# Performance work log

Measured on AMD Instinct MI355X. Metric: run time of the kernel, lower is better.

## Reference

```python
import jax, jax.numpy as jnp
import numpy as np


def _exp_levels(dx, depth):
    """Tensor-algebra exponential of a single increment dx [B, C]:
    level j is dx^{(x) j} / j!, flattened to [B, C^j]."""
    B = dx.shape[0]
    levels = [dx]
    for j in range(2, depth + 1):
        levels.append((jnp.einsum('bi,bj->bij', levels[-1], dx) / j).reshape(B, -1))
    return levels


def _chen_step(levels, dx, depth):
    """Chen's identity: sig(path * segment) = sig(path) (x) exp(dx).
    levels: tuple of [B, C^k] for k=1..depth. dx: [B, C]."""
    B = dx.shape[0]
    exps = _exp_levels(dx, depth)
    new = []
    for k in range(1, depth + 1):
        acc = levels[k - 1] + exps[k - 1]  # A_k * 1  +  1 * E_k
        for j in range(1, k):
            # A_{k-j} (x) E_j, flattened: [B, C^{k-j}] x [B, C^j] -> [B, C^k]
            acc = acc + jnp.einsum('bi,bj->bij', levels[k - j - 1], exps[j - 1]).reshape(B, -1)
        new.append(acc)
    return tuple(new)


def setup_inputs() -> dict:
    key = jax.random.key(0)
    path = jax.random.normal(key, (64, 512, 10), dtype=jnp.float32)
    return {"path": path, "depth": 4}


def reference(path, depth):
    # signature(path, depth, stream=False, basepoint=False, inverse=False,
    #           initial=None, scalar_term=False)
    dx = path[:, 1:] - path[:, :-1]  # [B, L-1, C] increments
    B = path.shape[0]
    # Initialise with the signature of the first segment: exp(dx_0).
    init = tuple(_exp_levels(dx[:, 0], depth))
    # Fold remaining segments via Chen's relation (a sequential scan; the
    # original's batch-trick is just a reassociation of this same product).
    dx_rest = jnp.swapaxes(dx[:, 1:], 0, 1)  # [L-2, B, C]

    def step(carry, d):
        return _chen_step(carry, d, depth), None

    carry, _ = jax.lax.scan(step, init, dx_rest)
    # Concatenate levels: output [B, C + C^2 + ... + C^depth]
    return jnp.concatenate(carry, axis=-1)
```

## Files before the change

### kernel.cpp

```cpp
#include <hip/hip_runtime.h>


#define CH      10
#define NSTEPS  511
#define SIGSZ   11110
#define WSSEG   11112
#define NSEG    8
#define SEGLEN  64
#define TRP     68

__global__ __launch_bounds__(256)
void sig_partial(const float* __restrict__ path, float* __restrict__ ws) {
    __shared__ __align__(16) float rowL[SEGLEN * 12];
    __shared__ __align__(16) float trL[CH * TRP];

    const int tid = threadIdx.x;
    const int bx  = blockIdx.x;
    const int b   = bx >> 3;
    const int seg = bx & 7;
    const int s0  = seg * SEGLEN;

    const float* p = path + (size_t)b * (512 * CH) + s0 * CH;
    for (int e = tid; e < SEGLEN * CH; e += 256) {
        const int s = e / CH;
        const int c = e - s * CH;
        float v = 0.f;
        if (s0 + s < NSTEPS) v = p[e + CH] - p[e];
        rowL[s * 12 + c] = v;
        trL[c * TRP + s] = v;
    }
    __syncthreads();

    const int half = tid >> 7;
    const int ij   = tid & 127;
    if (ij < 100) {
        const int ci = ij / 10;
        const int cj = ij - ci * 10;

        float a1 = 0.f, a2 = 0.f;
        float a3[5];
        float a4[5][10];
        #pragma unroll
        for (int m = 0; m < 5; ++m) {
            a3[m] = 0.f;
            #pragma unroll
            for (int l = 0; l < 10; ++l) a4[m][l] = 0.f;
        }

        const float* ti = trL + ci * TRP;
        const float* tj = trL + cj * TRP;

        auto run = [&](auto hc) {
            constexpr int H = decltype(hc)::value;
            for (int s4 = 0; s4 < SEGLEN; s4 += 4) {
                const float4 vi = *(const float4*)(ti + s4);
                const float4 vj = *(const float4*)(tj + s4);
                const float* rp = rowL + s4 * 12;
                #pragma unroll
                for (int u = 0; u < 4; ++u) {
                    const float4 d0 = *(const float4*)(rp + u * 12);
                    const float4 d1 = *(const float4*)(rp + u * 12 + 4);
                    const float2 d2 = *(const float2*)(rp + u * 12 + 8);
                    const float dxi = (u == 0) ? vi.x : (u == 1) ? vi.y
                                     : (u == 2) ? vi.z : vi.w;
                    const float dxj = (u == 0) ? vj.x : (u == 1) ? vj.y
                                     : (u == 2) ? vj.z : vj.w;

                    const float p1 = a1 * (1.f / 6.f) + dxi * (1.f / 24.f);
                    const float q1 = a1 * 0.5f        + dxi * (1.f / 6.f);
                    const float r1 = a1               + dxi * 0.5f;
                    const float p2 = a2 * 0.5f + p1 * dxj;
                    const float q2 = a2        + q1 * dxj;
                    a2 += r1 * dxj;
                    a1 += dxi;

                    const float dk0 = H ? d1.y : d0.x;
                    const float dk1 = H ? d1.z : d0.y;
                    const float dk2 = H ? d1.w : d0.z;
                    const float dk3 = H ? d2.x : d0.w;
                    const float dk4 = H ? d2.y : d1.x;

                    const float p30 = a3[0] + p2 * dk0;  a3[0] += q2 * dk0;
                    const float p31 = a3[1] + p2 * dk1;  a3[1] += q2 * dk1;
                    const float p32 = a3[2] + p2 * dk2;  a3[2] += q2 * dk2;
                    const float p33 = a3[3] + p2 * dk3;  a3[3] += q2 * dk3;
                    const float p34 = a3[4] + p2 * dk4;  a3[4] += q2 * dk4;

                    #pragma unroll
                    for (int m = 0; m < 5; ++m) {
                        const float p3 = (m == 0) ? p30 : (m == 1) ? p31
                                        : (m == 2) ? p32 : (m == 3) ? p33 : p34;
                        a4[m][0] += p3 * d0.x; a4[m][1] += p3 * d0.y;
                        a4[m][2] += p3 * d0.z; a4[m][3] += p3 * d0.w;
                        a4[m][4] += p3 * d1.x; a4[m][5] += p3 * d1.y;
                        a4[m][6] += p3 * d1.z; a4[m][7] += p3 * d1.w;
                        a4[m][8] += p3 * d2.x; a4[m][9] += p3 * d2.y;
                    }
                }
            }
        };
        if (half == 0) run(std::integral_constant<int, 0>{});
        else           run(std::integral_constant<int, 1>{});

        const int k0 = half * 5;
        float* ob = ws + (size_t)(b * NSEG + seg) * WSSEG;
        #pragma unroll
        for (int m = 0; m < 5; ++m) {
            const int id = ci * 100 + cj * 10 + k0 + m;
            float* o4 = ob + 1110 + id * 10;
            #pragma unroll
            for (int l = 0; l < 10; ++l) o4[l] = a4[m][l];
            ob[110 + id] = a3[m];
        }
        if (half == 0)            ob[10 + ci * 10 + cj] = a2;
        if (half == 0 && cj == 0) ob[ci] = a1;
    }
}

__global__ __launch_bounds__(256)
void sig_combine(const float* __restrict__ ws, float* __restrict__ out) {
    __shared__ float B[1110];

    const int tid  = threadIdx.x;
    const int b    = blockIdx.x >> 2;
    const int part = blockIdx.x & 3;
    const int id   = part * 256 + tid;
    const bool valid = (id < 1000);

    const int ci = id / 100;
    const int cj = (id / 10) % 10;
    const int ck = id % 10;

    const float* w0 = ws + (size_t)b * NSEG * WSSEG;

    float a1 = 0.f, a2 = 0.f, a3 = 0.f;
    float a4[10];
    #pragma unroll
    for (int l = 0; l < 10; ++l) a4[l] = 0.f;
    if (valid) {
        a1 = w0[ci];
        a2 = w0[10 + ci * 10 + cj];
        a3 = w0[110 + id];
        #pragma unroll
        for (int l = 0; l < 10; ++l) a4[l] = w0[1110 + id * 10 + l];
    }

    for (int s = 1; s < NSEG; ++s) {
        const float* wb = w0 + (size_t)s * WSSEG;
        __syncthreads();
        for (int e = tid; e < 1110; e += 256) B[e] = wb[e];
        __syncthreads();

        if (valid) {
            const float b1i   = B[ci];
            const float b1j   = B[cj];
            const float b1k   = B[ck];
            const float b2_ij = B[10 + ci * 10 + cj];
            const float b2_jk = B[10 + cj * 10 + ck];
            const float b3ijk = B[110 + id];

            float b4v[10];
            #pragma unroll
            for (int l = 0; l < 10; ++l) b4v[l] = wb[1110 + id * 10 + l];

            #pragma unroll
            for (int l = 0; l < 10; ++l)
                a4[l] += a3 * B[l] + a2 * B[10 + ck * 10 + l]
                       + a1 * B[110 + (cj * 10 + ck) * 10 + l] + b4v[l];
            a3 += a2 * b1k + a1 * b2_jk + b3ijk;
            a2 += a1 * b1j + b2_ij;
            a1 += b1i;
        }
    }

    if (valid) {
        float* ob = out + (size_t)b * SIGSZ;
        float* o4 = ob + 1110 + id * 10;
        #pragma unroll
        for (int l = 0; l < 10; ++l) o4[l] = a4[l];
        ob[110 + id] = a3;
        if (ck == 0)            ob[10 + ci * 10 + cj] = a2;
        if (ck == 0 && cj == 0) ob[ci] = a1;
    }
}

extern "C" void kernel_launch(void* const* d_in, const int* in_sizes, int n_in,
                              void* d_out, int out_size, void* d_ws, size_t ws_size,
                              hipStream_t stream) {
    const float* path = (const float*)d_in[0];
    float* out = (float*)d_out;
    float* ws  = (float*)d_ws;

    sig_partial<<<dim3(512), dim3(256), 0, stream>>>(path, ws);
    sig_combine<<<dim3(256), dim3(256), 0, stream>>>(ws, out);
}
```

Measured before the change: 97.36 us.

## Reassign partial-signature work to one (i,j,k) triple per thread with readlane broadcast

The partial kernel now splits each batch into 4 segments of 128 steps instead of 8 of 64, and splits the 1000 level-3 triples across 4 blocks so each thread owns a single (i,j,k) with 10 level-4 accumulators. Before, a thread held 5 triples with 50 accumulators. The row increments are loaded once per 32-step group into registers and broadcast through readlane, which avoids per-step LDS vector loads. The aim is fewer registers and higher occupancy, plus fewer combine steps. The cost is that each thread recomputes its level 1–2 prefix, the sequential chain per thread is longer, and readlane adds scalar-path overhead.

```diff
diff --git a/kernel.cpp b/kernel.cpp
--- a/kernel.cpp
+++ b/kernel.cpp
@@ -5,20 +5,28 @@
 #define NSTEPS  511
 #define SIGSZ   11110
 #define WSSEG   11112
-#define NSEG    8
-#define SEGLEN  64
-#define TRP     68
+#define NSEG    4
+#define SEGLEN  128
+#define TRP     132
+#define GSTEPS  32
+#define NGRP    (SEGLEN / GSTEPS)
+
+__device__ __forceinline__ float rl(float v, int lane) {
+    return __int_as_float(__builtin_amdgcn_readlane(__float_as_int(v), lane));
+}
 
 __global__ __launch_bounds__(256)
 void sig_partial(const float* __restrict__ path, float* __restrict__ ws) {
-    __shared__ __align__(16) float rowL[SEGLEN * 12];
+    __shared__ __align__(16) float flatL[SEGLEN * CH];
     __shared__ __align__(16) float trL[CH * TRP];
 
-    const int tid = threadIdx.x;
-    const int bx  = blockIdx.x;
-    const int b   = bx >> 3;
-    const int seg = bx & 7;
-    const int s0  = seg * SEGLEN;
+    const int tid  = threadIdx.x;
+    const int lane = tid & 63;
+    const int bx   = blockIdx.x;
+    const int b    = bx >> 4;
+    const int seg  = (bx >> 2) & 3;
+    const int part = bx & 3;
+    const int s0   = seg * SEGLEN;
 
     const float* p = path + (size_t)b * (512 * CH) + s0 * CH;
     for (int e = tid; e < SEGLEN * CH; e += 256) {
@@ -26,94 +34,81 @@
         const int c = e - s * CH;
         float v = 0.f;
         if (s0 + s < NSTEPS) v = p[e + CH] - p[e];
-        rowL[s * 12 + c] = v;
+        flatL[e] = v;
         trL[c * TRP + s] = v;
     }
     __syncthreads();
 
-    const int half = tid >> 7;
-    const int ij   = tid & 127;
-    if (ij < 100) {
-        const int ci = ij / 10;
-        const int cj = ij - ci * 10;
+    const int id  = part * 256 + tid;
+    const int idc = (id < 1000) ? id : 999;
+    const int ci = idc / 100;
+    const int cj = (idc / 10) % 10;
+    const int ck = idc % 10;
 
-        float a1 = 0.f, a2 = 0.f;
-        float a3[5];
-        float a4[5][10];
+    float a1 = 0.f, a2 = 0.f, a3 = 0.f;
+    float a4[10];
+    #pragma unroll
+    for (int l = 0; l < 10; ++l) a4[l] = 0.f;
+
+    const float* ti = trL + ci * TRP;
+    const float* tj = trL + cj * TRP;
+    const float* tk = trL + ck * TRP;
+
+    for (int g = 0; g < NGRP; ++g) {
+        const float* fb = flatL + g * (GSTEPS * CH);
+        const float f0 = fb[lane];
+        const float f1 = fb[64 + lane];
+        const float f2 = fb[128 + lane];
+        const float f3 = fb[192 + lane];
+        const float f4 = fb[256 + lane];
+        const int gs = g * GSTEPS;
+
         #pragma unroll
-        for (int m = 0; m < 5; ++m) {
-            a3[m] = 0.f;
+        for (int q = 0; q < GSTEPS / 4; ++q) {
+            const float4 vi = *(const float4*)(ti + gs + q * 4);
+            const float4 vj = *(const float4*)(tj + gs + q * 4);
+            const float4 vk = *(const float4*)(tk + gs + q * 4);
             #pragma unroll
-            for (int l = 0; l < 10; ++l) a4[m][l] = 0.f;
-        }
+            for (int u = 0; u < 4; ++u) {
+                const int sl = q * 4 + u;
+                const float dxi = (u == 0) ? vi.x : (u == 1) ? vi.y
+                                 : (u == 2) ? vi.z : vi.w;
+                const float dxj = (u == 0) ? vj.x : (u == 1) ? vj.y
+                                 : (u == 2) ? vj.z : vj.w;
+                const float dxk = (u == 0) ? vk.x : (u == 1) ? vk.y
+                                 : (u == 2) ? vk.z : vk.w;
 
-        const float* ti = trL + ci * TRP;
-        const float* tj = trL + cj * TRP;
+                const float p1 = a1 * (1.f / 6.f) + dxi * (1.f / 24.f);
+                const float q1 = a1 * 0.5f        + dxi * (1.f / 6.f);
+                const float r1 = a1               + dxi * 0.5f;
+                const float p2 = a2 * 0.5f + p1 * dxj;
+                const float q2 = a2        + q1 * dxj;
+                a2 += r1 * dxj;
+                const float p3 = a3 + p2 * dxk;
+                a3 += q2 * dxk;
+                a1 += dxi;
 
-        auto run = [&](auto hc) {
-            constexpr int H = decltype(hc)::value;
-            for (int s4 = 0; s4 < SEGLEN; s4 += 4) {
-                const float4 vi = *(const float4*)(ti + s4);
-                const float4 vj = *(const float4*)(tj + s4);
-                const float* rp = rowL + s4 * 12;
                 #pragma unroll
-                for (int u = 0; u < 4; ++u) {
-                    const float4 d0 = *(const float4*)(rp + u * 12);
-                    const float4 d1 = *(const float4*)(rp + u * 12 + 4);
-                    const float2 d2 = *(const float2*)(rp + u * 12 + 8);
-                    const float dxi = (u == 0) ? vi.x : (u == 1) ? vi.y
-                                     : (u == 2) ? vi.z : vi.w;
-                    const float dxj = (u == 0) ? vj.x : (u == 1) ? vj.y
-                                     : (u == 2) ? vj.z : vj.w;
-
-                    const float p1 = a1 * (1.f / 6.f) + dxi * (1.f / 24.f);
-                    const float q1 = a1 * 0.5f        + dxi * (1.f / 6.f);
-                    const float r1 = a1               + dxi * 0.5f;
-                    const float p2 = a2 * 0.5f + p1 * dxj;
-                    const float q2 = a2        + q1 * dxj;
-                    a2 += r1 * dxj;
-                    a1 += dxi;
-
-                    const float dk0 = H ? d1.y : d0.x;
-                    const float dk1 = H ? d1.z : d0.y;
-                    const float dk2 = H ? d1.w : d0.z;
-                    const float dk3 = H ? d2.x : d0.w;
-                    const float dk4 = H ? d2.y : d1.x;
-
-                    const float p30 = a3[0] + p2 * dk0;  a3[0] += q2 * dk0;
-                    const float p31 = a3[1] + p2 * dk1;  a3[1] += q2 * dk1;
-                    const float p32 = a3[2] + p2 * dk2;  a3[2] += q2 * dk2;
-                    const float p33 = a3[3] + p2 * dk3;  a3[3] += q2 * dk3;
-                    const float p34 = a3[4] + p2 * dk4;  a3[4] += q2 * dk4;
-
-                    #pragma unroll
-                    for (int m = 0; m < 5; ++m) {
-                        const float p3 = (m == 0) ? p30 : (m == 1) ? p31
-                                        : (m == 2) ? p32 : (m == 3) ? p33 : p34;
-                        a4[m][0] += p3 * d0.x; a4[m][1] += p3 * d0.y;
-                        a4[m][2] += p3 * d0.z; a4[m][3] += p3 * d0.w;
-                        a4[m][4] += p3 * d1.x; a4[m][5] += p3 * d1.y;
-                        a4[m][6] += p3 * d1.z; a4[m][7] += p3 * d1.w;
-                        a4[m][8] += p3 * d2.x; a4[m][9] += p3 * d2.y;
-                    }
+                for (int l = 0; l < 10; ++l) {
+                    const int idx = sl * 10 + l;
+                    const float fs = ((idx >> 6) == 0) ? f0
+                                   : ((idx >> 6) == 1) ? f1
+                                   : ((idx >> 6) == 2) ? f2
+                                   : ((idx >> 6) == 3) ? f3 : f4;
+                    a4[l] += p3 * rl(fs, idx & 63);
                 }
             }
-        };
-        if (half == 0) run(std::integral_constant<int, 0>{});
-        else           run(std::integral_constant<int, 1>{});
+        }
+    }
 
-        const int k0 = half * 5;
+    if (id < 1000) {
         float* ob = ws + (size_t)(b * NSEG + seg) * WSSEG;
+        float* o4 = ob + 1110 + id * 10;
         #pragma unroll
-        for (int m = 0; m < 5; ++m) {
-            const int id = ci * 100 + cj * 10 + k0 + m;
-            float* o4 = ob + 1110 + id * 10;
-            #pragma unroll
-            for (int l = 0; l < 10; ++l) o4[l] = a4[m][l];
-            ob[110 + id] = a3[m];
-        }
-        if (half == 0)            ob[10 + ci * 10 + cj] = a2;
-        if (half == 0 && cj == 0) ob[ci] = a1;
+        for (int l = 0; l < 10; ++l) o4[l] = a4[l];
+        ob[110 + id] = a3;
+        if (ck == 0)            ob[10 + ci * 10 + cj] = a2;
+        if (ck == 0 && cj == 0) ob[ci] = a1;
     }
 }
 
@@ -191,6 +186,6 @@
     float* out = (float*)d_out;
     float* ws  = (float*)d_ws;
 
-    sig_partial<<<dim3(512), dim3(256), 0, stream>>>(path, ws);
-    sig_combine<<<dim3(256), dim3(256), 0, stream>>>(ws, out);
+    sig_partial<<<dim3(1024), dim3(256), 0, stream>>>(path, ws);
+    sig_combine<<<dim3(256),  dim3(256), 0, stream>>>(ws, out);
 }
```

After: 100.3 us. +3.0%, slower.
